# Performance work log

Measured on AMD Instinct MI355X. Metric: run time of the kernel, lower is better.

The kernel has to match this reference:

```python
import jax, jax.numpy as jnp
import numpy as np

MARGIN = 0.3  # init kwarg, mode='norm'


def _pairwise_dist(X):
    # squared euclidean distances, then safe sqrt (matches euc_dist(X.t()).sqrt())
    sq = jnp.sum(X * X, axis=1)                      # [n]
    d2 = sq[:, None] + sq[None, :] - 2.0 * (X @ X.T)  # [n, n]
    d2 = jnp.maximum(d2, 0.0)
    # safe sqrt: avoid inf derivative at 0 (diagonal); forward value identical
    return jnp.where(d2 > 0.0, jnp.sqrt(jnp.where(d2 > 0.0, d2, 1.0)), 0.0)


def setup_inputs() -> dict:
    key = jax.random.key(0)
    kx, ky = jax.random.split(key)
    X = jax.random.normal(kx, (4096, 2048), dtype=jnp.float32)
    Y = jax.random.randint(ky, (4096,), 0, 128, dtype=jnp.int64)
    return {"X": X, "Y": Y}


def reference(X, Y):
    dist = _pairwise_dist(X)                         # [n, n]
    mask = Y[:, None] == Y[None, :]                  # same-identity mask [n, n]
    inf = jnp.array(jnp.inf, dtype=dist.dtype)
    # hardest positive per anchor: max over same-label entries
    dist_ap = jnp.max(jnp.where(mask, dist, -inf), axis=1)  # [n]
    # hardest negative per anchor: min over different-label entries
    dist_an = jnp.min(jnp.where(mask, inf, dist), axis=1)   # [n]
    # mode == 'norm': mean hinge
    return jnp.mean(jnp.maximum(dist_ap - dist_an + MARGIN, 0.0))
```

## Files before the change

### kernel.cpp

```cpp
#include <hip/hip_runtime.h>
#include <hip/hip_bf16.h>
#include <hip/hip_fp8.h>

typedef __attribute__((ext_vector_type(4))) int i32x4;
typedef __attribute__((ext_vector_type(8))) int i32x8;
typedef __attribute__((ext_vector_type(16))) float f32x16;

#define MARGIN 0.3f
#define BIGF 3.0e38f

__device__ __forceinline__ void gl2lds16(const void* g, void* l) {
    __builtin_amdgcn_global_load_lds(
        (const __attribute__((address_space(1))) void*)g,
        (__attribute__((address_space(3))) void*)l,
        16, 0, 0);
}

__global__ __launch_bounds__(256) void convert_norm_kernel(
    const float* __restrict__ X, unsigned char* __restrict__ Xq,
    float* __restrict__ nrm, unsigned* __restrict__ ap,
    unsigned* __restrict__ an, unsigned* __restrict__ cnt, int K) {
    const int wave = threadIdx.x >> 6, lane = threadIdx.x & 63;
    const int row = blockIdx.x * 4 + wave;
    const float* xr = X + (size_t)row * K;
    unsigned char* xqr = Xq + (size_t)row * K;
    float s = 0.0f;
    for (int c = lane * 8; c < K; c += 64 * 8) {
        float4 v0 = *(const float4*)(xr + c);
        float4 v1 = *(const float4*)(xr + c + 4);
        float f[8] = {v0.x, v0.y, v0.z, v0.w, v1.x, v1.y, v1.z, v1.w};
        union { unsigned char b[8]; uint2 u; } p;
#pragma unroll
        for (int i = 0; i < 8; i++) {
            __hip_fp8_e4m3 q(f[i]);
            p.b[i] = q.__x;
            float d = (float)q;
            s += d * d;
        }
        *(uint2*)(xqr + c) = p.u;
    }
    for (int off = 32; off > 0; off >>= 1) s += __shfl_xor(s, off, 64);
    if (lane == 0) {
        nrm[row] = s;
        ap[row] = 0u;
        an[row] = 0x7F800000u;
        if (row == 0) *cnt = 0u;
    }
}

__global__ __launch_bounds__(256, 4) void gemm_reduce_kernel(
    const unsigned char* __restrict__ Xq, const float* __restrict__ nrm,
    const int* __restrict__ Y, unsigned* __restrict__ ap,
    unsigned* __restrict__ an, unsigned* __restrict__ cnt,
    float* __restrict__ out, int N, int K) {
    __shared__ __align__(16) unsigned char sA[128 * 128];
    __shared__ __align__(16) unsigned char sB[128 * 128];
    __shared__ int sYr[128], sYc[128];
    __shared__ float sNr[128], sNc[128];
    __shared__ float redmax[4][64], redmin[4][64];
    __shared__ float lsum[4];
    __shared__ unsigned s_done;

    const int tid = threadIdx.x;
    const int wave = tid >> 6;
    const int lane = tid & 63;
    const int m = lane & 31;
    const int h = lane >> 5;
    const int wr = wave >> 1;
    const int wc = wave & 1;

    const int NB = N >> 7;
    const int rowBase = (blockIdx.x >> 5) * 128;
    const int colBase = (blockIdx.x & (NB - 1)) * 128;

    if (tid < 128) {
        sYr[tid] = Y[rowBase + tid];
        sNr[tid] = nrm[rowBase + tid];
    } else {
        int t = tid - 128;
        sYc[t] = Y[colBase + t];
        sNc[t] = nrm[colBase + t];
    }

    f32x16 acc[2][2];
#pragma unroll
    for (int si = 0; si < 2; si++)
#pragma unroll
        for (int sj = 0; sj < 2; sj++)
#pragma unroll
            for (int rr = 0; rr < 16; rr++) acc[si][sj][rr] = 0.0f;

    const int rsub = lane >> 3;
    const int jchunk = (lane & 7) ^ rsub;
    const unsigned char* gA = Xq + (size_t)(rowBase + wave * 32 + rsub) * K + jchunk * 16;
    const unsigned char* gB = Xq + (size_t)(colBase + wave * 32 + rsub) * K + jchunk * 16;
    unsigned char* lA = sA + wave * 4096;
    unsigned char* lB = sB + wave * 4096;
    const size_t g8 = (size_t)8 * K;

    const int e = m & 7;
    const int nit = K >> 7;

    for (int it = 0; it < nit; it++) {
        const size_t go = (size_t)it * 128;
#pragma unroll
        for (int g = 0; g < 4; g++) {
            gl2lds16(gA + go + g * g8, lA + g * 1024);
            gl2lds16(gB + go + g * g8, lB + g * 1024);
        }
        __syncthreads();

#pragma unroll
        for (int s = 0; s < 2; s++) {
            const int c0 = s * 4 + h * 2;
            i32x8 af[2], bf[2];
#pragma unroll
            for (int si = 0; si < 2; si++) {
                const unsigned char* base = sA + (wr * 64 + si * 32 + m) * 128;
                i32x4 lo = *(const i32x4*)(base + ((c0 ^ e) * 16));
                i32x4 hi = *(const i32x4*)(base + (((c0 + 1) ^ e) * 16));
                af[si] = __builtin_shufflevector(lo, hi, 0, 1, 2, 3, 4, 5, 6, 7);
            }
#pragma unroll
            for (int sj = 0; sj < 2; sj++) {
                const unsigned char* base = sB + (wc * 64 + sj * 32 + m) * 128;
                i32x4 lo = *(const i32x4*)(base + ((c0 ^ e) * 16));
                i32x4 hi = *(const i32x4*)(base + (((c0 + 1) ^ e) * 16));
                bf[sj] = __builtin_shufflevector(lo, hi, 0, 1, 2, 3, 4, 5, 6, 7);
            }
#pragma unroll
            for (int si = 0; si < 2; si++)
#pragma unroll
                for (int sj = 0; sj < 2; sj++)
                    acc[si][sj] = __builtin_amdgcn_mfma_scale_f32_32x32x64_f8f6f4(
                        af[si], bf[sj], acc[si][sj], 0 ,
                        0 , 0, 127 ,
                        0, 127 );
        }
        __syncthreads();
    }

#pragma unroll
    for (int si = 0; si < 2; si++)
#pragma unroll
        for (int reg = 0; reg < 16; reg++) {
            const int row64 = si * 32 + (reg & 3) + 8 * (reg >> 2) + 4 * h;
            const int rIdx = wr * 64 + row64;
            const int yr = sYr[rIdx];
            const float nr = sNr[rIdx];
            float dp = -1.0f, dn = BIGF;
#pragma unroll
            for (int sj = 0; sj < 2; sj++) {
                const int cIdx = wc * 64 + sj * 32 + m;
                float d2 = nr + sNc[cIdx] - 2.0f * acc[si][sj][reg];
                float d = sqrtf(fmaxf(d2, 0.0f));
                bool same = (yr == sYc[cIdx]);
                dp = fmaxf(dp, same ? d : -1.0f);
                dn = fminf(dn, same ? BIGF : d);
            }
            for (int off = 1; off < 32; off <<= 1) {
                dp = fmaxf(dp, __shfl_xor(dp, off, 64));
                dn = fminf(dn, __shfl_xor(dn, off, 64));
            }
            if (m == 0) {
                redmax[wave][row64] = dp;
                redmin[wave][row64] = dn;
            }
        }
    __syncthreads();

    if (tid < 128) {
        const int wr2 = tid >> 6, r64 = tid & 63;
        float mx = fmaxf(redmax[wr2 * 2][r64], redmax[wr2 * 2 + 1][r64]);
        float mn = fminf(redmin[wr2 * 2][r64], redmin[wr2 * 2 + 1][r64]);
        atomicMax(&ap[rowBase + tid], __float_as_uint(fmaxf(mx, 0.0f)));
        atomicMin(&an[rowBase + tid], __float_as_uint(mn));
    }

    __syncthreads();
    if (tid == 0) {
        __threadfence();
        s_done = atomicAdd(cnt, 1u);
    }
    __syncthreads();
    if (s_done == gridDim.x - 1) {
        __threadfence();
        float s = 0.0f;
        for (int i = tid; i < N; i += 256) {
            unsigned ua = __hip_atomic_load(&ap[i], __ATOMIC_RELAXED,
                                            __HIP_MEMORY_SCOPE_AGENT);
            unsigned ub = __hip_atomic_load(&an[i], __ATOMIC_RELAXED,
                                            __HIP_MEMORY_SCOPE_AGENT);
            s += fmaxf(__uint_as_float(ua) - __uint_as_float(ub) + MARGIN, 0.0f);
        }
        for (int off = 32; off > 0; off >>= 1) s += __shfl_xor(s, off, 64);
        if (lane == 0) lsum[wave] = s;
        __syncthreads();
        if (tid == 0)
            out[0] = (lsum[0] + lsum[1] + lsum[2] + lsum[3]) / (float)N;
    }
}

extern "C" void kernel_launch(void* const* d_in, const int* in_sizes, int n_in,
                              void* d_out, int out_size, void* d_ws, size_t ws_size,
                              hipStream_t stream) {
    const float* X = (const float*)d_in[0];
    const int* Y = (const int*)d_in[1];
    float* out = (float*)d_out;
    const int N = in_sizes[1];
    const int K = in_sizes[0] / N;

    char* ws = (char*)d_ws;
    unsigned char* Xq = (unsigned char*)ws;
    float* nrm = (float*)(ws + (size_t)N * K);
    unsigned* ap = (unsigned*)((char*)nrm + (size_t)N * 4);
    unsigned* an = (unsigned*)((char*)ap + (size_t)N * 4);
    unsigned* cnt = (unsigned*)((char*)an + (size_t)N * 4);

    convert_norm_kernel<<<N / 4, 256, 0, stream>>>(X, Xq, nrm, ap, an, cnt, K);
    const int NB = N / 128;
    gemm_reduce_kernel<<<NB * NB, 256, 0, stream>>>(Xq, nrm, Y, ap, an, cnt,
                                                    out, N, K);
}
```

Measured before the change: 133.2 us.

## Exploit distance symmetry: compute upper-triangular tiles only, reduce rows and columns

The GEMM grid now covers only the upper-triangular block pairs (NB*(NB+1)/2 tiles) instead of all NB*NB. Each tile also reduces hardest positive and negative along its columns and applies them through atomics to the column indices, which exploits the symmetry of the distance matrix. The fp32-to-fp8 conversion kernel also switches to packed cvt builtins when they are available. This roughly halves the MFMA work at the cost of an extra column reduction, more atomics, and a serial loop that decodes the triangular block index.

```diff
diff --git a/kernel.cpp b/kernel.cpp
--- a/kernel.cpp
+++ b/kernel.cpp
@@ -2,12 +2,20 @@
 #include <hip/hip_bf16.h>
 #include <hip/hip_fp8.h>
 
+typedef __attribute__((ext_vector_type(2))) float f32x2;
 typedef __attribute__((ext_vector_type(4))) int i32x4;
 typedef __attribute__((ext_vector_type(8))) int i32x8;
 typedef __attribute__((ext_vector_type(16))) float f32x16;
 
 #define MARGIN 0.3f
 #define BIGF 3.0e38f
+
+#if defined(__has_builtin)
+#if __has_builtin(__builtin_amdgcn_cvt_pk_fp8_f32) && \
+    __has_builtin(__builtin_amdgcn_cvt_pk_f32_fp8)
+#define HAVE_PK_FP8 1
+#endif
+#endif
 
 __device__ __forceinline__ void gl2lds16(const void* g, void* l) {
     __builtin_amdgcn_global_load_lds(
@@ -28,6 +36,21 @@
     for (int c = lane * 8; c < K; c += 64 * 8) {
         float4 v0 = *(const float4*)(xr + c);
         float4 v1 = *(const float4*)(xr + c + 4);
+#if defined(HAVE_PK_FP8)
+        int w0 = 0, w1 = 0;
+        w0 = __builtin_amdgcn_cvt_pk_fp8_f32(v0.x, v0.y, w0, false);
+        w0 = __builtin_amdgcn_cvt_pk_fp8_f32(v0.z, v0.w, w0, true);
+        w1 = __builtin_amdgcn_cvt_pk_fp8_f32(v1.x, v1.y, w1, false);
+        w1 = __builtin_amdgcn_cvt_pk_fp8_f32(v1.z, v1.w, w1, true);
+        f32x2 d0 = __builtin_amdgcn_cvt_pk_f32_fp8(w0, false);
+        f32x2 d1 = __builtin_amdgcn_cvt_pk_f32_fp8(w0, true);
+        f32x2 d2 = __builtin_amdgcn_cvt_pk_f32_fp8(w1, false);
+        f32x2 d3 = __builtin_amdgcn_cvt_pk_f32_fp8(w1, true);
+        s += d0[0]*d0[0] + d0[1]*d0[1] + d1[0]*d1[0] + d1[1]*d1[1];
+        s += d2[0]*d2[0] + d2[1]*d2[1] + d3[0]*d3[0] + d3[1]*d3[1];
+        uint2 u; u.x = (unsigned)w0; u.y = (unsigned)w1;
+        *(uint2*)(xqr + c) = u;
+#else
         float f[8] = {v0.x, v0.y, v0.z, v0.w, v1.x, v1.y, v1.z, v1.w};
         union { unsigned char b[8]; uint2 u; } p;
 #pragma unroll
@@ -38,6 +61,7 @@
             s += d * d;
         }
         *(uint2*)(xqr + c) = p.u;
+#endif
     }
     for (int off = 32; off > 0; off >>= 1) s += __shfl_xor(s, off, 64);
     if (lane == 0) {
@@ -58,6 +82,7 @@
     __shared__ int sYr[128], sYc[128];
     __shared__ float sNr[128], sNc[128];
     __shared__ float redmax[4][64], redmin[4][64];
+    __shared__ float credmax[2][2][64], credmin[2][2][64];
     __shared__ float lsum[4];
     __shared__ unsigned s_done;
 
@@ -69,9 +94,14 @@
     const int wr = wave >> 1;
     const int wc = wave & 1;
 
-    const int NB = N >> 7;
-    const int rowBase = (blockIdx.x >> 5) * 128;
-    const int colBase = (blockIdx.x & (NB - 1)) * 128;
+    int j = 0;
+    {
+        const int b = blockIdx.x;
+        while ((j + 1) * (j + 2) / 2 <= b) j++;
+    }
+    const int r = blockIdx.x - j * (j + 1) / 2;
+    const int rowBase = r * 128;
+    const int colBase = j * 128;
 
     if (tid < 128) {
         sYr[tid] = Y[rowBase + tid];
@@ -140,6 +170,8 @@
         __syncthreads();
     }
 
+    float cmx0 = -1.0f, cmx1 = -1.0f, cmn0 = BIGF, cmn1 = BIGF;
+
 #pragma unroll
     for (int si = 0; si < 2; si++)
 #pragma unroll
@@ -149,14 +181,25 @@
             const int yr = sYr[rIdx];
             const float nr = sNr[rIdx];
             float dp = -1.0f, dn = BIGF;
-#pragma unroll
-            for (int sj = 0; sj < 2; sj++) {
-                const int cIdx = wc * 64 + sj * 32 + m;
-                float d2 = nr + sNc[cIdx] - 2.0f * acc[si][sj][reg];
+            {
+                const int cIdx = wc * 64 + m;
+                float d2 = nr + sNc[cIdx] - 2.0f * acc[si][0][reg];
                 float d = sqrtf(fmaxf(d2, 0.0f));
                 bool same = (yr == sYc[cIdx]);
-                dp = fmaxf(dp, same ? d : -1.0f);
-                dn = fminf(dn, same ? BIGF : d);
+                float p = same ? d : -1.0f;
+                float n = same ? BIGF : d;
+                dp = fmaxf(dp, p); dn = fminf(dn, n);
+                cmx0 = fmaxf(cmx0, p); cmn0 = fminf(cmn0, n);
+            }
+            {
+                const int cIdx = wc * 64 + 32 + m;
+                float d2 = nr + sNc[cIdx] - 2.0f * acc[si][1][reg];
+                float d = sqrtf(fmaxf(d2, 0.0f));
+                bool same = (yr == sYc[cIdx]);
+                float p = same ? d : -1.0f;
+                float n = same ? BIGF : d;
+                dp = fmaxf(dp, p); dn = fminf(dn, n);
+                cmx1 = fmaxf(cmx1, p); cmn1 = fminf(cmn1, n);
             }
             for (int off = 1; off < 32; off <<= 1) {
                 dp = fmaxf(dp, __shfl_xor(dp, off, 64));
@@ -167,14 +210,27 @@
                 redmin[wave][row64] = dn;
             }
         }
+
+    {
+        float mx = fmaxf(cmx0, __shfl_xor(cmx0, 32, 64));
+        float mn = fminf(cmn0, __shfl_xor(cmn0, 32, 64));
+        if (h == 0) { credmax[wr][wc][m] = mx; credmin[wr][wc][m] = mn; }
+        mx = fmaxf(cmx1, __shfl_xor(cmx1, 32, 64));
+        mn = fminf(cmn1, __shfl_xor(cmn1, 32, 64));
+        if (h == 0) { credmax[wr][wc][32 + m] = mx; credmin[wr][wc][32 + m] = mn; }
+    }
     __syncthreads();
 
     if (tid < 128) {
-        const int wr2 = tid >> 6, r64 = tid & 63;
-        float mx = fmaxf(redmax[wr2 * 2][r64], redmax[wr2 * 2 + 1][r64]);
-        float mn = fminf(redmin[wr2 * 2][r64], redmin[wr2 * 2 + 1][r64]);
+        const int g2 = tid >> 6, i64 = tid & 63;
+        float mx = fmaxf(redmax[g2 * 2][i64], redmax[g2 * 2 + 1][i64]);
+        float mn = fminf(redmin[g2 * 2][i64], redmin[g2 * 2 + 1][i64]);
         atomicMax(&ap[rowBase + tid], __float_as_uint(fmaxf(mx, 0.0f)));
         atomicMin(&an[rowBase + tid], __float_as_uint(mn));
+        float cx = fmaxf(credmax[0][g2][i64], credmax[1][g2][i64]);
+        float cn = fminf(credmin[0][g2][i64], credmin[1][g2][i64]);
+        atomicMax(&ap[colBase + tid], __float_as_uint(fmaxf(cx, 0.0f)));
+        atomicMin(&an[colBase + tid], __float_as_uint(cn));
     }
 
     __syncthreads();
@@ -219,6 +275,7 @@
 
     convert_norm_kernel<<<N / 4, 256, 0, stream>>>(X, Xq, nrm, ap, an, cnt, K);
     const int NB = N / 128;
-    gemm_reduce_kernel<<<NB * NB, 256, 0, stream>>>(Xq, nrm, Y, ap, an, cnt,
+    const int nblocks = NB * (NB + 1) / 2;
+    gemm_reduce_kernel<<<nblocks, 256, 0, stream>>>(Xq, nrm, Y, ap, an, cnt,
                                                     out, N, K);
 }
```

Result: no change. 133.4 us (+0.1%).
